# Performance work log

Hardware: AMD Instinct MI355X
Metric: run time of the kernel (lower is better)

Reference implementation:

```python
import jax, jax.numpy as jnp
import numpy as np

EPS = 1e-5

def bn(x, g, b, m, v):
    # inference-mode BatchNorm2d over channel dim
    return (x - m[None, :, None, None]) * jax.lax.rsqrt(v[None, :, None, None] + EPS) * g[None, :, None, None] + b[None, :, None, None]

def conv1x1(x, W, b=None):
    y = jnp.einsum('oc,bchw->bohw', W, x)
    return y + b[None, :, None, None] if b is not None else y

def forward(x, W3, b3, g1, b1, m1, v1, Wa, ba, g2, b2, m2, v2, Wq, bq, Wk, bk, Wv, bv, gam, Wg, bg, g3, b3n, m3, v3, Wf, bf, g4, b4, m4, v4, Wr, rs):
    B, C, H, Wd = x.shape
    N = H * Wd
    # conv branch: 3x3 conv + BN + ReLU
    y3 = jax.lax.conv_general_dilated(x, W3, (1, 1), ((1, 1), (1, 1)), dimension_numbers=('NCHW', 'OIHW', 'NCHW'))
    local = jax.nn.relu(bn(y3 + b3[None, :, None, None], g1, b1, m1, v1))
    # attn branch: 1x1 conv + BN + ReLU, then full-resolution attention
    a = jax.nn.relu(bn(conv1x1(x, Wa, ba), g2, b2, m2, v2))
    q = conv1x1(a, Wq, bq).reshape(B, -1, N)   # [B, C/8, N]
    k = conv1x1(a, Wk, bk).reshape(B, -1, N)   # [B, C/8, N]
    v = conv1x1(a, Wv, bv).reshape(B, -1, N)   # [B, C, N]
    att = jax.nn.softmax(jnp.einsum('bcn,bcm->bnm', q, k), axis=-1)  # [B, N, N], unscaled as in source
    o = jnp.einsum('bcm,bnm->bcn', v, att).reshape(a.shape)
    attn_feat = gam * o + a
    # gated fusion
    combined = jnp.concatenate([local, attn_feat], axis=1)
    gate = jax.nn.sigmoid(bn(conv1x1(combined, Wg, bg), g3, b3n, m3, v3))
    fused = gate * local + (1.0 - gate) * attn_feat
    out = jax.nn.relu(bn(conv1x1(jnp.concatenate([fused, combined], axis=1), Wf, bf), g4, b4, m4, v4))
    res = conv1x1(x, Wr)  # residual 1x1 conv, no bias (in != out channels)
    return out + rs * res

def setup_inputs() -> dict:
    B, Ci, Co, H, W_ = 4, 64, 128, 64, 64
    Cq = Co // 8
    ks = jax.random.split(jax.random.key(0), 24)
    def rn(i, s, sc=0.05):
        return jax.random.normal(ks[i], s, jnp.float32) * sc
    def var(i, c):
        return jax.random.uniform(ks[i], (c,), jnp.float32, 0.5, 1.5)
    ones = lambda c: jnp.ones((c,), jnp.float32)
    zeros = lambda c: jnp.zeros((c,), jnp.float32)
    return {
        'x': rn(0, (B, Ci, H, W_), 1.0),
        'W3': rn(1, (Co, Ci, 3, 3)), 'b3': rn(2, (Co,)),
        'g1': ones(Co), 'b1': zeros(Co), 'm1': rn(3, (Co,), 0.1), 'v1': var(4, Co),
        'Wa': rn(5, (Co, Ci)), 'ba': rn(6, (Co,)),
        'g2': ones(Co), 'b2': zeros(Co), 'm2': rn(7, (Co,), 0.1), 'v2': var(8, Co),
        'Wq': rn(9, (Cq, Co)), 'bq': rn(10, (Cq,)),
        'Wk': rn(11, (Cq, Co)), 'bk': rn(12, (Cq,)),
        'Wv': rn(13, (Co, Co)), 'bv': rn(14, (Co,)),
        'gam': jnp.array(0.5, jnp.float32),
        'Wg': rn(15, (Co, 2 * Co)), 'bg': rn(16, (Co,)),
        'g3': ones(Co), 'b3n': zeros(Co), 'm3': rn(17, (Co,), 0.1), 'v3': var(18, Co),
        'Wf': rn(19, (Co, 3 * Co)), 'bf': rn(20, (Co,)),
        'g4': ones(Co), 'b4': zeros(Co), 'm4': rn(21, (Co,), 0.1), 'v4': var(22, Co),
        'Wr': rn(23, (Co, Ci)),
        'rs': jnp.array(0.1, jnp.float32),
    }

def reference(x, W3, b3, g1, b1, m1, v1, Wa, ba, g2, b2, m2, v2, Wq, bq, Wk, bk, Wv, bv, gam, Wg, bg, g3, b3n, m3, v3, Wf, bf, g4, b4, m4, v4, Wr, rs):
    return forward(x, W3, b3, g1, b1, m1, v1, Wa, ba, g2, b2, m2, v2, Wq, bq, Wk, bk, Wv, bv, gam, Wg, bg, g3, b3n, m3, v3, Wf, bf, g4, b4, m4, v4, Wr, rs)
```

## Files before the change

kernel.cpp:

```cpp
#include <hip/hip_runtime.h>
#include <hip/hip_bf16.h>

#define CI_ 64
#define CO_ 128
#define NPIX 4096
#define CQ_ 16
#define EPS_ 1e-5f

typedef __attribute__((ext_vector_type(8))) __bf16 bf16x8;
typedef __attribute__((ext_vector_type(4))) __bf16 bf16x4;
typedef __attribute__((ext_vector_type(4))) float f32x4;

__global__ __launch_bounds__(256) void z_prepx(
    const float* __restrict__ x, __bf16* __restrict__ xT)
{
    __shared__ float tl[64][65];
    int b = blockIdx.x >> 6;
    int n0 = (blockIdx.x & 63) * 64;
    int tid = threadIdx.x;
    int nn = tid & 63, c4 = tid >> 6;
#pragma unroll
    for (int p = 0; p < 16; ++p) {
        int ci = p * 4 + c4;
        tl[ci][nn] = x[((size_t)b * CI_ + ci) * NPIX + n0 + nn];
    }
    __syncthreads();
#pragma unroll
    for (int p = 0; p < 2; ++p) {
        int idx = p * 256 + tid;
        int n = idx >> 3, cig = idx & 7;
        bf16x8 vv;
#pragma unroll
        for (int j = 0; j < 8; ++j) vv[j] = (__bf16)tl[cig * 8 + j][n];
        ((bf16x8*)xT)[((size_t)b * NPIX + n0 + n) * 8 + cig] = vv;
    }
}

__global__ __launch_bounds__(256) void z_prepw2(
    const float* __restrict__ W3, __bf16* __restrict__ Wt2,
    const float* __restrict__ Wg, const float* __restrict__ Wf, const float* __restrict__ Wr,
    const float* __restrict__ Wa, const float* __restrict__ Wq, const float* __restrict__ Wk,
    const float* __restrict__ Wv, __bf16* __restrict__ Wb)
{
    int i = blockIdx.x * 256 + threadIdx.x;
    if (i < 73728) {
        int co = i / 576;
        int r = i - co * 576;
        int tap = r >> 6;
        int ci = r & 63;
        Wt2[i] = (__bf16)W3[((size_t)co * CI_ + ci) * 9 + tap];
    }
    if (i < 118784) {
        float val;
        if (i < 32768) val = Wg[i];
        else if (i < 81920) val = Wf[i - 32768];
        else if (i < 90112) val = Wr[i - 81920];
        else if (i < 98304) val = Wa[i - 90112];
        else if (i < 100352) val = Wq[i - 98304];
        else if (i < 102400) val = Wk[i - 100352];
        else val = Wv[i - 102400];
        Wb[i] = (__bf16)val;
    }
}

__global__ __launch_bounds__(256) void z_mega(
    const __bf16* __restrict__ xT, const __bf16* __restrict__ Wb,
    const float* __restrict__ ba, const float* __restrict__ g2, const float* __restrict__ b2,
    const float* __restrict__ m2, const float* __restrict__ v2,
    const float* __restrict__ bq, const float* __restrict__ bk, const float* __restrict__ bv,
    float* __restrict__ a, float* __restrict__ q, __bf16* __restrict__ kT, __bf16* __restrict__ V2)
{
    __shared__ __align__(16) __bf16 an[16 * 128];
    int tid = threadIdx.x;
    int b = blockIdx.x >> 8;
    int n0 = (blockIdx.x & 255) * 16;
    int l = tid & 63, w = tid >> 6;
    int lm = l & 15, g = l >> 4;

    const __bf16* Wa2 = Wb + 90112;
    const __bf16* Wq2 = Wb + 98304;
    const __bf16* Wk2 = Wb + 100352;
    const __bf16* Wv2 = Wb + 102400;

    bf16x8 bx[2];
#pragma unroll
    for (int kc = 0; kc < 2; ++kc)
        bx[kc] = ((const bf16x8*)xT)[((size_t)b * NPIX + n0 + lm) * 8 + (kc * 4 + g)];
    f32x4 pa[2];
#pragma unroll
    for (int ct = 0; ct < 2; ++ct) {
#pragma unroll
        for (int r = 0; r < 4; ++r) pa[ct][r] = ba[w * 32 + ct * 16 + g * 4 + r];
#pragma unroll
        for (int kc = 0; kc < 2; ++kc) {
            bf16x8 afr = *(const bf16x8*)&Wa2[(size_t)(w * 32 + ct * 16 + lm) * 64 + kc * 32 + g * 8];
            pa[ct] = __builtin_amdgcn_mfma_f32_16x16x32_bf16(afr, bx[kc], pa[ct], 0, 0, 0);
        }
    }
#pragma unroll
    for (int ct = 0; ct < 2; ++ct) {
        bf16x4 pk;
#pragma unroll
        for (int r = 0; r < 4; ++r) {
            int co = w * 32 + ct * 16 + g * 4 + r;
            float sc = rsqrtf(v2[co] + EPS_) * g2[co];
            float sh = b2[co] - m2[co] * sc;
            float y = fmaxf(pa[ct][r] * sc + sh, 0.f);
            a[((size_t)b * CO_ + co) * NPIX + n0 + lm] = y;
            pk[r] = (__bf16)y;
        }
        int co8 = w * 4 + ct * 2 + (g >> 1);
        int ch = co8 ^ (lm & 7);
        *(bf16x4*)&an[lm * 128 + ch * 8 + (g & 1) * 4] = pk;
    }
    __syncthreads();

    bf16x8 bn[4];
#pragma unroll
    for (int kc = 0; kc < 4; ++kc) {
        int ch = (kc * 4 + g) ^ (lm & 7);
        bn[kc] = *(const bf16x8*)&an[lm * 128 + ch * 8];
    }
    f32x4 pv[2];
#pragma unroll
    for (int ct = 0; ct < 2; ++ct) {
#pragma unroll
        for (int r = 0; r < 4; ++r) pv[ct][r] = bv[w * 32 + ct * 16 + g * 4 + r];
#pragma unroll
        for (int kc = 0; kc < 4; ++kc) {
            bf16x8 afr = *(const bf16x8*)&Wv2[(size_t)(w * 32 + ct * 16 + lm) * 128 + kc * 32 + g * 8];
            pv[ct] = __builtin_amdgcn_mfma_f32_16x16x32_bf16(afr, bn[kc], pv[ct], 0, 0, 0);
        }
    }
    int n = n0 + lm;
#pragma unroll
    for (int ct = 0; ct < 2; ++ct)
#pragma unroll
        for (int r = 0; r < 4; ++r) {
            int c = w * 32 + ct * 16 + g * 4 + r;
            V2[(size_t)b * 524288 + (size_t)(n >> 3) * 1024 + c * 8 + (n & 7)] = (__bf16)pv[ct][r];
        }
    if (w == 0) {
        f32x4 pq;
#pragma unroll
        for (int r = 0; r < 4; ++r) pq[r] = bq[g * 4 + r];
#pragma unroll
        for (int kc = 0; kc < 4; ++kc) {
            bf16x8 afr = *(const bf16x8*)&Wq2[(size_t)lm * 128 + kc * 32 + g * 8];
            pq = __builtin_amdgcn_mfma_f32_16x16x32_bf16(afr, bn[kc], pq, 0, 0, 0);
        }
#pragma unroll
        for (int r = 0; r < 4; ++r)
            q[((size_t)b * CQ_ + g * 4 + r) * NPIX + n] = pq[r];
    } else if (w == 1) {
        f32x4 pk2;
#pragma unroll
        for (int r = 0; r < 4; ++r) pk2[r] = bk[g * 4 + r];
#pragma unroll
        for (int kc = 0; kc < 4; ++kc) {
            bf16x8 afr = *(const bf16x8*)&Wk2[(size_t)lm * 128 + kc * 32 + g * 8];
            pk2 = __builtin_amdgcn_mfma_f32_16x16x32_bf16(afr, bn[kc], pk2, 0, 0, 0);
        }
        bf16x4 kk;
#pragma unroll
        for (int r = 0; r < 4; ++r) kk[r] = (__bf16)pk2[r];
        *(bf16x4*)&kT[((size_t)b * NPIX + n) * CQ_ + g * 4] = kk;
    }
}

__global__ __launch_bounds__(256) void z_conv3mb(
    const __bf16* __restrict__ xT, const __bf16* __restrict__ Wt2,
    const float* __restrict__ b3, const float* __restrict__ g,
    const float* __restrict__ bb, const float* __restrict__ m,
    const float* __restrict__ v, __bf16* __restrict__ local_bf)
{
    __shared__ __align__(16) __bf16 xt[3 * 66 * 64];
    __shared__ __align__(16) __bf16 wt[32 * 576];
    __shared__ float scs[32], shs[32];

    int blk = blockIdx.x;
    int b = blk >> 8;
    int h = (blk >> 2) & 63;
    int cg = blk & 3;
    int co0 = cg * 32;
    int tid = threadIdx.x;
    int l = tid & 63;
    int nt = tid >> 6;
    int lm = l & 15, lh = l >> 4;

    if (tid < 32) {
        int co = co0 + tid;
        float scv = rsqrtf(v[co] + EPS_) * g[co];
        scs[tid] = scv;
        shs[tid] = (b3[co] - m[co]) * scv + bb[co];
    }

    const bf16x8* xs = (const bf16x8*)xT + (size_t)b * (NPIX * 8);
    for (int i = tid; i < 1584; i += 256) {
        int r = i / 528;
        int rem = i - r * 528;
        int c = rem >> 3;
        int cig = rem & 7;
        int hh = h + r - 1;
        int gc = c - 1;
        bf16x8 val;
#pragma unroll
        for (int j = 0; j < 8; ++j) val[j] = (__bf16)0.f;
        if ((unsigned)hh < 64u && (unsigned)gc < 64u)
            val = xs[(hh * 64 + gc) * 8 + cig];
        *(bf16x8*)&xt[(r * 66 + c) * 64 + ((cig ^ (c & 7)) * 8)] = val;
    }
    const bf16x8* wsrc = (const bf16x8*)Wt2 + (size_t)co0 * 72;
    for (int i = tid; i < 2304; i += 256) {
        int co = i / 72;
        int kc = i - co * 72;
        *(bf16x8*)&wt[co * 576 + ((kc ^ (co & 7)) * 8)] = wsrc[i];
    }
    __syncthreads();

    f32x4 acc0 = {0.f, 0.f, 0.f, 0.f};
    f32x4 acc1 = {0.f, 0.f, 0.f, 0.f};
#pragma unroll
    for (int tap = 0; tap < 9; ++tap) {
        int dh = tap / 3, dw = tap % 3;
#pragma unroll
        for (int ks = 0; ks < 2; ++ks) {
            int cig = ks * 4 + lh;
            int col = nt * 16 + lm + dw;
            bf16x8 bfr = *(const bf16x8*)&xt[(dh * 66 + col) * 64 + ((cig ^ (col & 7)) * 8)];
            int kcg = tap * 8 + cig;
            bf16x8 a0 = *(const bf16x8*)&wt[lm * 576 + ((kcg ^ (lm & 7)) * 8)];
            bf16x8 a1 = *(const bf16x8*)&wt[(16 + lm) * 576 + ((kcg ^ (lm & 7)) * 8)];
            acc0 = __builtin_amdgcn_mfma_f32_16x16x32_bf16(a0, bfr, acc0, 0, 0, 0);
            acc1 = __builtin_amdgcn_mfma_f32_16x16x32_bf16(a1, bfr, acc1, 0, 0, 0);
        }
    }

    size_t obase = (size_t)b * CO_ * NPIX + h * 64 + nt * 16 + lm;
#pragma unroll
    for (int r = 0; r < 4; ++r) {
        int cl0 = lh * 4 + r;
        float y0 = fmaxf(acc0[r] * scs[cl0] + shs[cl0], 0.f);
        local_bf[obase + (size_t)(co0 + cl0) * NPIX] = (__bf16)y0;
        int cl1 = 16 + cl0;
        float y1 = fmaxf(acc1[r] * scs[cl1] + shs[cl1], 0.f);
        local_bf[obase + (size_t)(co0 + cl1) * NPIX] = (__bf16)y1;
    }
}

__global__ __launch_bounds__(256) void z_attn8(
    const float* __restrict__ q, const __bf16* __restrict__ kT, const __bf16* __restrict__ V2,
    __bf16* __restrict__ o_part, float2* __restrict__ ml)
{
    __shared__ __align__(16) unsigned char smem[16896];
    __shared__ float wmaxA[4][16], wsumA[4][16], fsA[16];
    __shared__ float wmaxB[4][16], wsumB[4][16], fsB[16];
    __bf16* pA = (__bf16*)smem;
    __bf16* pB = (__bf16*)(smem + 8448);
    float* o_lds = (float*)smem;

    int tid = threadIdx.x;
    int b = blockIdx.x >> 8;
    int half = (blockIdx.x >> 7) & 1;
    int q0 = (blockIdx.x & 127) * 32;
    int l = tid & 63;
    int w = tid >> 6;
    int lm = l & 15;
    int g = l >> 4;

    bf16x8 qfA, qfB;
#pragma unroll
    for (int j = 0; j < 8; ++j) { qfA[j] = (__bf16)0.f; qfB[j] = (__bf16)0.f; }
    if (g < 2) {
#pragma unroll
        for (int j = 0; j < 8; ++j) {
            qfA[j] = (__bf16)q[((size_t)b * CQ_ + g * 8 + j) * NPIX + q0 + lm];
            qfB[j] = (__bf16)q[((size_t)b * CQ_ + g * 8 + j) * NPIX + q0 + 16 + lm];
        }
    }

    float mA = -1e30f, lA = 0.f, mB = -1e30f, lB = 0.f;
    f32x4 aA0 = {0.f,0.f,0.f,0.f}, aA1 = {0.f,0.f,0.f,0.f};
    f32x4 aB0 = {0.f,0.f,0.f,0.f}, aB1 = {0.f,0.f,0.f,0.f};
    int c0 = w * 32 + lm;
    int c1 = c0 + 16;
    const bf16x8* vbase = (const bf16x8*)V2 + (size_t)b * 65536;
    const __bf16* ktb = kT + (size_t)b * NPIX * CQ_;

    for (int t = 0; t < 8; ++t) {
        int m0 = half * 2048 + t * 256;
        {
            f32x4 sfr[4];
#pragma unroll
            for (int ms = 0; ms < 4; ++ms) {
                bf16x8 kf;
#pragma unroll
                for (int j = 0; j < 8; ++j) kf[j] = (__bf16)0.f;
                if (g < 2)
                    kf = *(const bf16x8*)&ktb[(size_t)(m0 + w * 64 + ms * 16 + lm) * CQ_ + g * 8];
                f32x4 zz = {0.f, 0.f, 0.f, 0.f};
                sfr[ms] = __builtin_amdgcn_mfma_f32_16x16x32_bf16(kf, qfA, zz, 0, 0, 0);
            }
            float pmax = -1e30f;
#pragma unroll
            for (int ms = 0; ms < 4; ++ms)
#pragma unroll
                for (int r = 0; r < 4; ++r) pmax = fmaxf(pmax, sfr[ms][r]);
            pmax = fmaxf(pmax, __shfl_xor(pmax, 16));
            pmax = fmaxf(pmax, __shfl_xor(pmax, 32));
            if (g == 0) wmaxA[w][lm] = pmax;
            __syncthreads();
            float tmax = fmaxf(fmaxf(wmaxA[0][lm], wmaxA[1][lm]), fmaxf(wmaxA[2][lm], wmaxA[3][lm]));
            float nm = fmaxf(mA, tmax);
            float f = __expf(mA - nm);
            mA = nm;
            if (w == 0 && g == 0) fsA[lm] = f;
            float psum = 0.f;
#pragma unroll
            for (int ms = 0; ms < 4; ++ms) {
                float p0 = __expf(sfr[ms][0] - nm);
                float p1 = __expf(sfr[ms][1] - nm);
                float p2 = __expf(sfr[ms][2] - nm);
                float p3 = __expf(sfr[ms][3] - nm);
                psum += (p0 + p1) + (p2 + p3);
                bf16x4 pk;
                pk[0] = (__bf16)p0; pk[1] = (__bf16)p1; pk[2] = (__bf16)p2; pk[3] = (__bf16)p3;
                *(bf16x4*)&pA[lm * 264 + w * 64 + ms * 16 + g * 4] = pk;
            }
            psum += __shfl_xor(psum, 16);
            psum += __shfl_xor(psum, 32);
            if (g == 0) wsumA[w][lm] = psum;
            __syncthreads();
            float tsum = (wsumA[0][lm] + wsumA[1][lm]) + (wsumA[2][lm] + wsumA[3][lm]);
            lA = lA * f + tsum;
        }
        {
            f32x4 sfr[4];
#pragma unroll
            for (int ms = 0; ms < 4; ++ms) {
                bf16x8 kf;
#pragma unroll
                for (int j = 0; j < 8; ++j) kf[j] = (__bf16)0.f;
                if (g < 2)
                    kf = *(const bf16x8*)&ktb[(size_t)(m0 + w * 64 + ms * 16 + lm) * CQ_ + g * 8];
                f32x4 zz = {0.f, 0.f, 0.f, 0.f};
                sfr[ms] = __builtin_amdgcn_mfma_f32_16x16x32_bf16(kf, qfB, zz, 0, 0, 0);
            }
            float pmax = -1e30f;
#pragma unroll
            for (int ms = 0; ms < 4; ++ms)
#pragma unroll
                for (int r = 0; r < 4; ++r) pmax = fmaxf(pmax, sfr[ms][r]);
            pmax = fmaxf(pmax, __shfl_xor(pmax, 16));
            pmax = fmaxf(pmax, __shfl_xor(pmax, 32));
            if (g == 0) wmaxB[w][lm] = pmax;
            __syncthreads();
            float tmax = fmaxf(fmaxf(wmaxB[0][lm], wmaxB[1][lm]), fmaxf(wmaxB[2][lm], wmaxB[3][lm]));
            float nm = fmaxf(mB, tmax);
            float f = __expf(mB - nm);
            mB = nm;
            if (w == 0 && g == 0) fsB[lm] = f;
            float psum = 0.f;
#pragma unroll
            for (int ms = 0; ms < 4; ++ms) {
                float p0 = __expf(sfr[ms][0] - nm);
                float p1 = __expf(sfr[ms][1] - nm);
                float p2 = __expf(sfr[ms][2] - nm);
                float p3 = __expf(sfr[ms][3] - nm);
                psum += (p0 + p1) + (p2 + p3);
                bf16x4 pk;
                pk[0] = (__bf16)p0; pk[1] = (__bf16)p1; pk[2] = (__bf16)p2; pk[3] = (__bf16)p3;
                *(bf16x4*)&pB[lm * 264 + w * 64 + ms * 16 + g * 4] = pk;
            }
            psum += __shfl_xor(psum, 16);
            psum += __shfl_xor(psum, 32);
            if (g == 0) wsumB[w][lm] = psum;
            __syncthreads();
            float tsum = (wsumB[0][lm] + wsumB[1][lm]) + (wsumB[2][lm] + wsumB[3][lm]);
            lB = lB * f + tsum;
        }
        {
            float fA0 = fsA[g * 4 + 0], fA1 = fsA[g * 4 + 1], fA2 = fsA[g * 4 + 2], fA3 = fsA[g * 4 + 3];
            float fB0 = fsB[g * 4 + 0], fB1 = fsB[g * 4 + 1], fB2 = fsB[g * 4 + 2], fB3 = fsB[g * 4 + 3];
            aA0[0] *= fA0; aA0[1] *= fA1; aA0[2] *= fA2; aA0[3] *= fA3;
            aA1[0] *= fA0; aA1[1] *= fA1; aA1[2] *= fA2; aA1[3] *= fA3;
            aB0[0] *= fB0; aB0[1] *= fB1; aB0[2] *= fB2; aB0[3] *= fB3;
            aB1[0] *= fB0; aB1[1] *= fB1; aB1[2] *= fB2; aB1[3] *= fB3;
#pragma unroll
            for (int ks = 0; ks < 8; ++ks) {
                int msv = (m0 >> 3) + ks * 4 + g;
                bf16x8 bf0 = vbase[msv * 128 + c0];
                bf16x8 bf1 = vbase[msv * 128 + c1];
                bf16x8 afA = *(const bf16x8*)&pA[lm * 264 + ks * 32 + g * 8];
                bf16x8 afB = *(const bf16x8*)&pB[lm * 264 + ks * 32 + g * 8];
                aA0 = __builtin_amdgcn_mfma_f32_16x16x32_bf16(afA, bf0, aA0, 0, 0, 0);
                aA1 = __builtin_amdgcn_mfma_f32_16x16x32_bf16(afA, bf1, aA1, 0, 0, 0);
                aB0 = __builtin_amdgcn_mfma_f32_16x16x32_bf16(afB, bf0, aB0, 0, 0, 0);
                aB1 = __builtin_amdgcn_mfma_f32_16x16x32_bf16(afB, bf1, aB1, 0, 0, 0);
            }
        }
    }

    __syncthreads();
#pragma unroll
    for (int r = 0; r < 4; ++r) {
        int qrow = g * 4 + r;
        o_lds[c0 * 17 + qrow] = aA0[r];
        o_lds[c1 * 17 + qrow] = aA1[r];
    }
    if (w == 0 && g == 0)
        ml[(size_t)(half * 4 + b) * NPIX + q0 + lm] = make_float2(mA, lA);
    __syncthreads();
    {
        int qi = tid & 15;
        float inv = 1.f / lA;
#pragma unroll
        for (int j = 0; j < 8; ++j) {
            int cc = (tid >> 4) + 16 * j;
            size_t idx = ((size_t)(half * 4 + b) * CO_ + cc) * NPIX + q0 + qi;
            o_part[idx] = (__bf16)(o_lds[cc * 17 + qi] * inv);
        }
    }
    __syncthreads();
#pragma unroll
    for (int r = 0; r < 4; ++r) {
        int qrow = g * 4 + r;
        o_lds[c0 * 17 + qrow] = aB0[r];
        o_lds[c1 * 17 + qrow] = aB1[r];
    }
    if (w == 0 && g == 0)
        ml[(size_t)(half * 4 + b) * NPIX + q0 + 16 + lm] = make_float2(mB, lB);
    __syncthreads();
    {
        int qi = tid & 15;
        float inv = 1.f / lB;
#pragma unroll
        for (int j = 0; j < 8; ++j) {
            int cc = (tid >> 4) + 16 * j;
            size_t idx = ((size_t)(half * 4 + b) * CO_ + cc) * NPIX + q0 + 16 + qi;
            o_part[idx] = (__bf16)(o_lds[cc * 17 + qi] * inv);
        }
    }
}

__global__ __launch_bounds__(256) void z_fuseout3(
    const __bf16* __restrict__ local_bf, const __bf16* __restrict__ o_part,
    const float2* __restrict__ ml, const float* __restrict__ a,
    const float* __restrict__ gamp, const __bf16* __restrict__ xT,
    const __bf16* __restrict__ Wb,
    const float* __restrict__ bg, const float* __restrict__ g3, const float* __restrict__ b3n,
    const float* __restrict__ m3, const float* __restrict__ v3,
    const float* __restrict__ bfb, const float* __restrict__ g4, const float* __restrict__ b4,
    const float* __restrict__ m4, const float* __restrict__ v4,
    const float* __restrict__ rsp, float* __restrict__ out)
{
    __shared__ __align__(16) unsigned char smem[32768 + 4096];
    __shared__ float wA[32], wB[32];
    __bf16* sb2 = (__bf16*)smem;
    __bf16* sxT = (__bf16*)(smem + 28672);

    int tid = threadIdx.x;
    int b = blockIdx.x >> 7;
    int n0 = (blockIdx.x & 127) * 32;

    if (tid < 32) {
        float2 m1 = ml[(size_t)b * NPIX + n0 + tid];
        float2 m2 = ml[(size_t)(4 + b) * NPIX + n0 + tid];
        float mm = fmaxf(m1.x, m2.x);
        float w1 = m1.y * __expf(m1.x - mm);
        float w2 = m2.y * __expf(m2.x - mm);
        float inv = 1.f / (w1 + w2);
        wA[tid] = w1 * inv;
        wB[tid] = w2 * inv;
    }
    __syncthreads();

    float gam = gamp[0];
#pragma unroll
    for (int p = 0; p < 4; ++p) {
        int idx = p * 256 + tid;
        int c = idx >> 3, j = idx & 7;
        bf16x4 lv = *(const bf16x4*)&local_bf[((size_t)b * CO_ + c) * NPIX + n0 + j * 4];
        bf16x4 o1 = *(const bf16x4*)&o_part[((size_t)b * CO_ + c) * NPIX + n0 + j * 4];
        bf16x4 o2 = *(const bf16x4*)&o_part[((size_t)(4 + b) * CO_ + c) * NPIX + n0 + j * 4];
        float av[4];
        *(float4*)av = *(const float4*)(a + ((size_t)b * CO_ + c) * NPIX + n0 + j * 4);
#pragma unroll
        for (int e = 0; e < 4; ++e) {
            int n = j * 4 + e;
            int k1 = 128 + c, k2 = 256 + c;
            sb2[n * 448 + (((k1 >> 3) ^ (n & 7)) << 3) + (k1 & 7)] = lv[e];
            float o = (float)o1[e] * wA[n] + (float)o2[e] * wB[n];
            sb2[n * 448 + (((k2 >> 3) ^ (n & 7)) << 3) + (k2 & 7)] = (__bf16)(gam * o + av[e]);
        }
    }
#pragma unroll
    for (int p = 0; p < 2; ++p) {
        int idx = p * 256 + tid;
        int n = idx >> 3, cig = idx & 7;
        bf16x8 vv = ((const bf16x8*)xT)[((size_t)b * NPIX + n0 + n) * 8 + cig];
        *(bf16x8*)&sxT[n * 64 + ((cig ^ (n & 7)) << 3)] = vv;
    }
    __syncthreads();

    int l = tid & 63, w = tid >> 6;
    int lm = l & 15, g = l >> 4;
    int co0 = w * 32;
    int t7 = lm & 7;

    f32x4 p1[2][2];
#pragma unroll
    for (int cs = 0; cs < 2; ++cs) {
        float bv = bg[co0 + cs * 16 + lm];
#pragma unroll
        for (int ns = 0; ns < 2; ++ns) {
            p1[ns][cs][0] = bv; p1[ns][cs][1] = bv; p1[ns][cs][2] = bv; p1[ns][cs][3] = bv;
        }
    }
    const __bf16* Wg2 = Wb;
#pragma unroll
    for (int kc = 0; kc < 8; ++kc) {
        int ch = (16 + kc * 4 + g) ^ t7;
        bf16x8 a0 = *(const bf16x8*)&sb2[lm * 448 + ch * 8];
        bf16x8 a1 = *(const bf16x8*)&sb2[(16 + lm) * 448 + ch * 8];
        bf16x8 b0 = *(const bf16x8*)&Wg2[(size_t)(co0 + lm) * 256 + kc * 32 + g * 8];
        bf16x8 b1 = *(const bf16x8*)&Wg2[(size_t)(co0 + 16 + lm) * 256 + kc * 32 + g * 8];
        p1[0][0] = __builtin_amdgcn_mfma_f32_16x16x32_bf16(a0, b0, p1[0][0], 0, 0, 0);
        p1[0][1] = __builtin_amdgcn_mfma_f32_16x16x32_bf16(a0, b1, p1[0][1], 0, 0, 0);
        p1[1][0] = __builtin_amdgcn_mfma_f32_16x16x32_bf16(a1, b0, p1[1][0], 0, 0, 0);
        p1[1][1] = __builtin_amdgcn_mfma_f32_16x16x32_bf16(a1, b1, p1[1][1], 0, 0, 0);
    }
#pragma unroll
    for (int cs = 0; cs < 2; ++cs) {
        int co = co0 + cs * 16 + lm;
        float sc3 = rsqrtf(v3[co] + EPS_) * g3[co];
        float sh3 = b3n[co] - m3[co] * sc3;
        int kl = 128 + co, ka = 256 + co;
#pragma unroll
        for (int ns = 0; ns < 2; ++ns)
#pragma unroll
            for (int r = 0; r < 4; ++r) {
                int n = ns * 16 + g * 4 + r;
                float z = p1[ns][cs][r] * sc3 + sh3;
                float gate = 1.f / (1.f + __expf(-z));
                float lv = (float)sb2[n * 448 + (((kl >> 3) ^ (n & 7)) << 3) + (kl & 7)];
                float av = (float)sb2[n * 448 + (((ka >> 3) ^ (n & 7)) << 3) + (ka & 7)];
                float fu = gate * lv + (1.f - gate) * av;
                sb2[n * 448 + (((co >> 3) ^ (n & 7)) << 3) + (co & 7)] = (__bf16)fu;
            }
    }
    __syncthreads();

    f32x4 p2[2][2], pr[2][2];
#pragma unroll
    for (int cs = 0; cs < 2; ++cs) {
        float bv = bfb[co0 + cs * 16 + lm];
#pragma unroll
        for (int ns = 0; ns < 2; ++ns) {
            p2[ns][cs][0] = bv; p2[ns][cs][1] = bv; p2[ns][cs][2] = bv; p2[ns][cs][3] = bv;
            pr[ns][cs] = (f32x4){0.f, 0.f, 0.f, 0.f};
        }
    }
    const __bf16* Wf2 = Wb + 32768;
    const __bf16* Wr2 = Wb + 81920;
#pragma unroll
    for (int kc = 0; kc < 12; ++kc) {
        int ch = (kc * 4 + g) ^ t7;
        bf16x8 a0 = *(const bf16x8*)&sb2[lm * 448 + ch * 8];
        bf16x8 a1 = *(const bf16x8*)&sb2[(16 + lm) * 448 + ch * 8];
        bf16x8 b0 = *(const bf16x8*)&Wf2[(size_t)(co0 + lm) * 384 + kc * 32 + g * 8];
        bf16x8 b1 = *(const bf16x8*)&Wf2[(size_t)(co0 + 16 + lm) * 384 + kc * 32 + g * 8];
        p2[0][0] = __builtin_amdgcn_mfma_f32_16x16x32_bf16(a0, b0, p2[0][0], 0, 0, 0);
        p2[0][1] = __builtin_amdgcn_mfma_f32_16x16x32_bf16(a0, b1, p2[0][1], 0, 0, 0);
        p2[1][0] = __builtin_amdgcn_mfma_f32_16x16x32_bf16(a1, b0, p2[1][0], 0, 0, 0);
        p2[1][1] = __builtin_amdgcn_mfma_f32_16x16x32_bf16(a1, b1, p2[1][1], 0, 0, 0);
    }
#pragma unroll
    for (int kc = 0; kc < 2; ++kc) {
        int ch = (kc * 4 + g) ^ t7;
        bf16x8 a0 = *(const bf16x8*)&sxT[lm * 64 + ch * 8];
        bf16x8 a1 = *(const bf16x8*)&sxT[(16 + lm) * 64 + ch * 8];
        bf16x8 b0 = *(const bf16x8*)&Wr2[(size_t)(co0 + lm) * 64 + kc * 32 + g * 8];
        bf16x8 b1 = *(const bf16x8*)&Wr2[(size_t)(co0 + 16 + lm) * 64 + kc * 32 + g * 8];
        pr[0][0] = __builtin_amdgcn_mfma_f32_16x16x32_bf16(a0, b0, pr[0][0], 0, 0, 0);
        pr[0][1] = __builtin_amdgcn_mfma_f32_16x16x32_bf16(a0, b1, pr[0][1], 0, 0, 0);
        pr[1][0] = __builtin_amdgcn_mfma_f32_16x16x32_bf16(a1, b0, pr[1][0], 0, 0, 0);
        pr[1][1] = __builtin_amdgcn_mfma_f32_16x16x32_bf16(a1, b1, pr[1][1], 0, 0, 0);
    }
    __syncthreads();

    float* o_lds = (float*)smem;
    float rsv = rsp[0];
#pragma unroll
    for (int cs = 0; cs < 2; ++cs) {
        int co = co0 + cs * 16 + lm;
        float sc4 = rsqrtf(v4[co] + EPS_) * g4[co];
        float sh4 = b4[co] - m4[co] * sc4;
#pragma unroll
        for (int ns = 0; ns < 2; ++ns)
#pragma unroll
            for (int r = 0; r < 4; ++r) {
                int n = ns * 16 + g * 4 + r;
                float o = fmaxf(p2[ns][cs][r] * sc4 + sh4, 0.f) + rsv * pr[ns][cs][r];
                o_lds[co * 36 + n] = o;
            }
    }
    __syncthreads();
    {
        int c = tid >> 1, h = tid & 1;
#pragma unroll
        for (int j2 = 0; j2 < 4; ++j2) {
            float4 vv = *(float4*)&o_lds[c * 36 + h * 16 + j2 * 4];
            *(float4*)(out + ((size_t)b * CO_ + c) * NPIX + n0 + h * 16 + j2 * 4) = vv;
        }
    }
}

extern "C" void kernel_launch(void* const* d_in, const int* in_sizes, int n_in,
                              void* d_out, int out_size, void* d_ws, size_t ws_size,
                              hipStream_t stream) {
    const float* x   = (const float*)d_in[0];
    const float* W3  = (const float*)d_in[1];
    const float* b3  = (const float*)d_in[2];
    const float* g1  = (const float*)d_in[3];
    const float* b1  = (const float*)d_in[4];
    const float* m1  = (const float*)d_in[5];
    const float* v1  = (const float*)d_in[6];
    const float* Wa  = (const float*)d_in[7];
    const float* ba  = (const float*)d_in[8];
    const float* g2  = (const float*)d_in[9];
    const float* b2  = (const float*)d_in[10];
    const float* m2  = (const float*)d_in[11];
    const float* v2  = (const float*)d_in[12];
    const float* Wq  = (const float*)d_in[13];
    const float* bq  = (const float*)d_in[14];
    const float* Wk  = (const float*)d_in[15];
    const float* bk  = (const float*)d_in[16];
    const float* Wv  = (const float*)d_in[17];
    const float* bv  = (const float*)d_in[18];
    const float* gam = (const float*)d_in[19];
    const float* Wg  = (const float*)d_in[20];
    const float* bg  = (const float*)d_in[21];
    const float* g3  = (const float*)d_in[22];
    const float* b3n = (const float*)d_in[23];
    const float* m3  = (const float*)d_in[24];
    const float* v3  = (const float*)d_in[25];
    const float* Wf  = (const float*)d_in[26];
    const float* bfb = (const float*)d_in[27];
    const float* g4  = (const float*)d_in[28];
    const float* b4  = (const float*)d_in[29];
    const float* m4  = (const float*)d_in[30];
    const float* v4  = (const float*)d_in[31];
    const float* Wr  = (const float*)d_in[32];
    const float* rs  = (const float*)d_in[33];

    float* ws      = (float*)d_ws;
    float* a_      = ws;
    __bf16* local_bf = (__bf16*)(ws + 2097152);
    __bf16* V2     = (__bf16*)(ws + 3145728);
    float* q       = ws + 4194304;
    __bf16* kT     = (__bf16*)(ws + 4456448);
    __bf16* xT     = (__bf16*)(ws + 4587520);
    __bf16* Wt2    = (__bf16*)(ws + 5111808);
    __bf16* Wb     = (__bf16*)(ws + 5152768);
    __bf16* o_part = (__bf16*)(ws + 5214208);
    float2* ml     = (float2*)(ws + 7311360);

    float* out = (float*)d_out;

    z_prepx<<<256, 256, 0, stream>>>(x, xT);
    z_prepw2<<<464, 256, 0, stream>>>(W3, Wt2, Wg, Wf, Wr, Wa, Wq, Wk, Wv, Wb);
    z_mega<<<1024, 256, 0, stream>>>(xT, Wb, ba, g2, b2, m2, v2, bq, bk, bv, a_, q, kT, V2);
    z_attn8<<<1024, 256, 0, stream>>>(q, kT, V2, o_part, ml);
    z_conv3mb<<<1024, 256, 0, stream>>>(xT, Wt2, b3, g1, b1, m1, v1, local_bf);
    z_fuseout3<<<512, 256, 0, stream>>>(local_bf, o_part, ml, a_, gam, xT, Wb,
                                        bg, g3, b3n, m3, v3, bfb, g4, b4, m4, v4, rs, out);
}
```

Before: 109.6 us.

## Use two-pass softmax with precomputed row max and store Q as bf16 transposed

The attention kernel now runs a first pass over all keys in its half to compute the exact row maximum of QK^T. A second pass computes the exponentials, accumulates P·V and sums the probabilities without any online rescaling. This removes the per-tile max/sum block reductions, most syncthreads and the accumulator rescale multiplies. The price is computing the QK^T MFMAs twice. Q is also written by the projection kernel as bf16 in a pixel-major layout, so each lane loads its fragment with one vector load instead of 16 strided fp32 loads.

```diff
diff --git a/kernel.cpp b/kernel.cpp
--- a/kernel.cpp
+++ b/kernel.cpp
@@ -68,7 +68,7 @@
     const float* __restrict__ ba, const float* __restrict__ g2, const float* __restrict__ b2,
     const float* __restrict__ m2, const float* __restrict__ v2,
     const float* __restrict__ bq, const float* __restrict__ bk, const float* __restrict__ bv,
-    float* __restrict__ a, float* __restrict__ q, __bf16* __restrict__ kT, __bf16* __restrict__ V2)
+    float* __restrict__ a, __bf16* __restrict__ qT, __bf16* __restrict__ kT, __bf16* __restrict__ V2)
 {
     __shared__ __align__(16) __bf16 an[16 * 128];
     int tid = threadIdx.x;
@@ -149,9 +149,10 @@
             bf16x8 afr = *(const bf16x8*)&Wq2[(size_t)lm * 128 + kc * 32 + g * 8];
             pq = __builtin_amdgcn_mfma_f32_16x16x32_bf16(afr, bn[kc], pq, 0, 0, 0);
         }
-#pragma unroll
-        for (int r = 0; r < 4; ++r)
-            q[((size_t)b * CQ_ + g * 4 + r) * NPIX + n] = pq[r];
+        bf16x4 qq;
+#pragma unroll
+        for (int r = 0; r < 4; ++r) qq[r] = (__bf16)pq[r];
+        *(bf16x4*)&qT[((size_t)b * NPIX + n) * CQ_ + g * 4] = qq;
     } else if (w == 1) {
         f32x4 pk2;
 #pragma unroll
@@ -248,13 +249,12 @@
     }
 }
 
-__global__ __launch_bounds__(256) void z_attn8(
-    const float* __restrict__ q, const __bf16* __restrict__ kT, const __bf16* __restrict__ V2,
+__global__ __launch_bounds__(256) void z_attn9(
+    const __bf16* __restrict__ qT, const __bf16* __restrict__ kT, const __bf16* __restrict__ V2,
     __bf16* __restrict__ o_part, float2* __restrict__ ml)
 {
     __shared__ __align__(16) unsigned char smem[16896];
-    __shared__ float wmaxA[4][16], wsumA[4][16], fsA[16];
-    __shared__ float wmaxB[4][16], wsumB[4][16], fsB[16];
+    __shared__ float wredA[4][16], wredB[4][16];
     __bf16* pA = (__bf16*)smem;
     __bf16* pB = (__bf16*)(smem + 8448);
     float* o_lds = (float*)smem;
@@ -271,137 +271,100 @@
     bf16x8 qfA, qfB;
 #pragma unroll
     for (int j = 0; j < 8; ++j) { qfA[j] = (__bf16)0.f; qfB[j] = (__bf16)0.f; }
+    const __bf16* qtb = qT + (size_t)b * NPIX * CQ_;
     if (g < 2) {
-#pragma unroll
-        for (int j = 0; j < 8; ++j) {
-            qfA[j] = (__bf16)q[((size_t)b * CQ_ + g * 8 + j) * NPIX + q0 + lm];
-            qfB[j] = (__bf16)q[((size_t)b * CQ_ + g * 8 + j) * NPIX + q0 + 16 + lm];
-        }
-    }
-
-    float mA = -1e30f, lA = 0.f, mB = -1e30f, lB = 0.f;
+        qfA = *(const bf16x8*)&qtb[(size_t)(q0 + lm) * CQ_ + g * 8];
+        qfB = *(const bf16x8*)&qtb[(size_t)(q0 + 16 + lm) * CQ_ + g * 8];
+    }
+
+    const bf16x8* vbase = (const bf16x8*)V2 + (size_t)b * 65536;
+    const __bf16* ktb = kT + (size_t)b * NPIX * CQ_;
+
+    float mxA = -1e30f, mxB = -1e30f;
+    for (int t = 0; t < 8; ++t) {
+        int m0 = half * 2048 + t * 256;
+#pragma unroll
+        for (int ms = 0; ms < 4; ++ms) {
+            bf16x8 kf;
+#pragma unroll
+            for (int j = 0; j < 8; ++j) kf[j] = (__bf16)0.f;
+            if (g < 2)
+                kf = *(const bf16x8*)&ktb[(size_t)(m0 + w * 64 + ms * 16 + lm) * CQ_ + g * 8];
+            f32x4 zz = {0.f, 0.f, 0.f, 0.f};
+            f32x4 sA = __builtin_amdgcn_mfma_f32_16x16x32_bf16(kf, qfA, zz, 0, 0, 0);
+            f32x4 sB = __builtin_amdgcn_mfma_f32_16x16x32_bf16(kf, qfB, zz, 0, 0, 0);
+#pragma unroll
+            for (int r = 0; r < 4; ++r) {
+                mxA = fmaxf(mxA, sA[r]);
+                mxB = fmaxf(mxB, sB[r]);
+            }
+        }
+    }
+    mxA = fmaxf(mxA, __shfl_xor(mxA, 16));
+    mxA = fmaxf(mxA, __shfl_xor(mxA, 32));
+    mxB = fmaxf(mxB, __shfl_xor(mxB, 16));
+    mxB = fmaxf(mxB, __shfl_xor(mxB, 32));
+    if (g == 0) { wredA[w][lm] = mxA; wredB[w][lm] = mxB; }
+    __syncthreads();
+    float MA = fmaxf(fmaxf(wredA[0][lm], wredA[1][lm]), fmaxf(wredA[2][lm], wredA[3][lm]));
+    float MB = fmaxf(fmaxf(wredB[0][lm], wredB[1][lm]), fmaxf(wredB[2][lm], wredB[3][lm]));
+
     f32x4 aA0 = {0.f,0.f,0.f,0.f}, aA1 = {0.f,0.f,0.f,0.f};
     f32x4 aB0 = {0.f,0.f,0.f,0.f}, aB1 = {0.f,0.f,0.f,0.f};
+    float sumA = 0.f, sumB = 0.f;
     int c0 = w * 32 + lm;
     int c1 = c0 + 16;
-    const bf16x8* vbase = (const bf16x8*)V2 + (size_t)b * 65536;
-    const __bf16* ktb = kT + (size_t)b * NPIX * CQ_;
 
     for (int t = 0; t < 8; ++t) {
         int m0 = half * 2048 + t * 256;
-        {
-            f32x4 sfr[4];
-#pragma unroll
-            for (int ms = 0; ms < 4; ++ms) {
-                bf16x8 kf;
-#pragma unroll
-                for (int j = 0; j < 8; ++j) kf[j] = (__bf16)0.f;
-                if (g < 2)
-                    kf = *(const bf16x8*)&ktb[(size_t)(m0 + w * 64 + ms * 16 + lm) * CQ_ + g * 8];
-                f32x4 zz = {0.f, 0.f, 0.f, 0.f};
-                sfr[ms] = __builtin_amdgcn_mfma_f32_16x16x32_bf16(kf, qfA, zz, 0, 0, 0);
-            }
-            float pmax = -1e30f;
-#pragma unroll
-            for (int ms = 0; ms < 4; ++ms)
-#pragma unroll
-                for (int r = 0; r < 4; ++r) pmax = fmaxf(pmax, sfr[ms][r]);
-            pmax = fmaxf(pmax, __shfl_xor(pmax, 16));
-            pmax = fmaxf(pmax, __shfl_xor(pmax, 32));
-            if (g == 0) wmaxA[w][lm] = pmax;
-            __syncthreads();
-            float tmax = fmaxf(fmaxf(wmaxA[0][lm], wmaxA[1][lm]), fmaxf(wmaxA[2][lm], wmaxA[3][lm]));
-            float nm = fmaxf(mA, tmax);
-            float f = __expf(mA - nm);
-            mA = nm;
-            if (w == 0 && g == 0) fsA[lm] = f;
-            float psum = 0.f;
-#pragma unroll
-            for (int ms = 0; ms < 4; ++ms) {
-                float p0 = __expf(sfr[ms][0] - nm);
-                float p1 = __expf(sfr[ms][1] - nm);
-                float p2 = __expf(sfr[ms][2] - nm);
-                float p3 = __expf(sfr[ms][3] - nm);
-                psum += (p0 + p1) + (p2 + p3);
-                bf16x4 pk;
-                pk[0] = (__bf16)p0; pk[1] = (__bf16)p1; pk[2] = (__bf16)p2; pk[3] = (__bf16)p3;
-                *(bf16x4*)&pA[lm * 264 + w * 64 + ms * 16 + g * 4] = pk;
-            }
-            psum += __shfl_xor(psum, 16);
-            psum += __shfl_xor(psum, 32);
-            if (g == 0) wsumA[w][lm] = psum;
-            __syncthreads();
-            float tsum = (wsumA[0][lm] + wsumA[1][lm]) + (wsumA[2][lm] + wsumA[3][lm]);
-            lA = lA * f + tsum;
-        }
-        {
-            f32x4 sfr[4];
-#pragma unroll
-            for (int ms = 0; ms < 4; ++ms) {
-                bf16x8 kf;
-#pragma unroll
-                for (int j = 0; j < 8; ++j) kf[j] = (__bf16)0.f;
-                if (g < 2)
-                    kf = *(const bf16x8*)&ktb[(size_t)(m0 + w * 64 + ms * 16 + lm) * CQ_ + g * 8];
-                f32x4 zz = {0.f, 0.f, 0.f, 0.f};
-                sfr[ms] = __builtin_amdgcn_mfma_f32_16x16x32_bf16(kf, qfB, zz, 0, 0, 0);
-            }
-            float pmax = -1e30f;
-#pragma unroll
-            for (int ms = 0; ms < 4; ++ms)
-#pragma unroll
-                for (int r = 0; r < 4; ++r) pmax = fmaxf(pmax, sfr[ms][r]);
-            pmax = fmaxf(pmax, __shfl_xor(pmax, 16));
-            pmax = fmaxf(pmax, __shfl_xor(pmax, 32));
-            if (g == 0) wmaxB[w][lm] = pmax;
-            __syncthreads();
-            float tmax = fmaxf(fmaxf(wmaxB[0][lm], wmaxB[1][lm]), fmaxf(wmaxB[2][lm], wmaxB[3][lm]));
-            float nm = fmaxf(mB, tmax);
-            float f = __expf(mB - nm);
-            mB = nm;
-            if (w == 0 && g == 0) fsB[lm] = f;
-            float psum = 0.f;
-#pragma unroll
-            for (int ms = 0; ms < 4; ++ms) {
-                float p0 = __expf(sfr[ms][0] - nm);
-                float p1 = __expf(sfr[ms][1] - nm);
-                float p2 = __expf(sfr[ms][2] - nm);
-                float p3 = __expf(sfr[ms][3] - nm);
-                psum += (p0 + p1) + (p2 + p3);
-                bf16x4 pk;
-                pk[0] = (__bf16)p0; pk[1] = (__bf16)p1; pk[2] = (__bf16)p2; pk[3] = (__bf16)p3;
-                *(bf16x4*)&pB[lm * 264 + w * 64 + ms * 16 + g * 4] = pk;
-            }
-            psum += __shfl_xor(psum, 16);
-            psum += __shfl_xor(psum, 32);
-            if (g == 0) wsumB[w][lm] = psum;
-            __syncthreads();
-            float tsum = (wsumB[0][lm] + wsumB[1][lm]) + (wsumB[2][lm] + wsumB[3][lm]);
-            lB = lB * f + tsum;
-        }
-        {
-            float fA0 = fsA[g * 4 + 0], fA1 = fsA[g * 4 + 1], fA2 = fsA[g * 4 + 2], fA3 = fsA[g * 4 + 3];
-            float fB0 = fsB[g * 4 + 0], fB1 = fsB[g * 4 + 1], fB2 = fsB[g * 4 + 2], fB3 = fsB[g * 4 + 3];
-            aA0[0] *= fA0; aA0[1] *= fA1; aA0[2] *= fA2; aA0[3] *= fA3;
-            aA1[0] *= fA0; aA1[1] *= fA1; aA1[2] *= fA2; aA1[3] *= fA3;
-            aB0[0] *= fB0; aB0[1] *= fB1; aB0[2] *= fB2; aB0[3] *= fB3;
-            aB1[0] *= fB0; aB1[1] *= fB1; aB1[2] *= fB2; aB1[3] *= fB3;
-#pragma unroll
-            for (int ks = 0; ks < 8; ++ks) {
-                int msv = (m0 >> 3) + ks * 4 + g;
-                bf16x8 bf0 = vbase[msv * 128 + c0];
-                bf16x8 bf1 = vbase[msv * 128 + c1];
-                bf16x8 afA = *(const bf16x8*)&pA[lm * 264 + ks * 32 + g * 8];
-                bf16x8 afB = *(const bf16x8*)&pB[lm * 264 + ks * 32 + g * 8];
-                aA0 = __builtin_amdgcn_mfma_f32_16x16x32_bf16(afA, bf0, aA0, 0, 0, 0);
-                aA1 = __builtin_amdgcn_mfma_f32_16x16x32_bf16(afA, bf1, aA1, 0, 0, 0);
-                aB0 = __builtin_amdgcn_mfma_f32_16x16x32_bf16(afB, bf0, aB0, 0, 0, 0);
-                aB1 = __builtin_amdgcn_mfma_f32_16x16x32_bf16(afB, bf1, aB1, 0, 0, 0);
-            }
-        }
-    }
-
-    __syncthreads();
+#pragma unroll
+        for (int ms = 0; ms < 4; ++ms) {
+            bf16x8 kf;
+#pragma unroll
+            for (int j = 0; j < 8; ++j) kf[j] = (__bf16)0.f;
+            if (g < 2)
+                kf = *(const bf16x8*)&ktb[(size_t)(m0 + w * 64 + ms * 16 + lm) * CQ_ + g * 8];
+            f32x4 zz = {0.f, 0.f, 0.f, 0.f};
+            f32x4 sA = __builtin_amdgcn_mfma_f32_16x16x32_bf16(kf, qfA, zz, 0, 0, 0);
+            f32x4 sB = __builtin_amdgcn_mfma_f32_16x16x32_bf16(kf, qfB, zz, 0, 0, 0);
+            float a0 = __expf(sA[0] - MA), a1 = __expf(sA[1] - MA);
+            float a2 = __expf(sA[2] - MA), a3 = __expf(sA[3] - MA);
+            sumA += (a0 + a1) + (a2 + a3);
+            bf16x4 pkA;
+            pkA[0] = (__bf16)a0; pkA[1] = (__bf16)a1; pkA[2] = (__bf16)a2; pkA[3] = (__bf16)a3;
+            *(bf16x4*)&pA[lm * 264 + w * 64 + ms * 16 + g * 4] = pkA;
+            float b0 = __expf(sB[0] - MB), b1 = __expf(sB[1] - MB);
+            float b2 = __expf(sB[2] - MB), b3 = __expf(sB[3] - MB);
+            sumB += (b0 + b1) + (b2 + b3);
+            bf16x4 pkB;
+            pkB[0] = (__bf16)b0; pkB[1] = (__bf16)b1; pkB[2] = (__bf16)b2; pkB[3] = (__bf16)b3;
+            *(bf16x4*)&pB[lm * 264 + w * 64 + ms * 16 + g * 4] = pkB;
+        }
+        __syncthreads();
+#pragma unroll
+        for (int ks = 0; ks < 8; ++ks) {
+            int msv = (m0 >> 3) + ks * 4 + g;
+            bf16x8 bf0 = vbase[msv * 128 + c0];
+            bf16x8 bf1 = vbase[msv * 128 + c1];
+            bf16x8 afA = *(const bf16x8*)&pA[lm * 264 + ks * 32 + g * 8];
+            bf16x8 afB = *(const bf16x8*)&pB[lm * 264 + ks * 32 + g * 8];
+            aA0 = __builtin_amdgcn_mfma_f32_16x16x32_bf16(afA, bf0, aA0, 0, 0, 0);
+            aA1 = __builtin_amdgcn_mfma_f32_16x16x32_bf16(afA, bf1, aA1, 0, 0, 0);
+            aB0 = __builtin_amdgcn_mfma_f32_16x16x32_bf16(afB, bf0, aB0, 0, 0, 0);
+            aB1 = __builtin_amdgcn_mfma_f32_16x16x32_bf16(afB, bf1, aB1, 0, 0, 0);
+        }
+        __syncthreads();
+    }
+
+    sumA += __shfl_xor(sumA, 16);
+    sumA += __shfl_xor(sumA, 32);
+    sumB += __shfl_xor(sumB, 16);
+    sumB += __shfl_xor(sumB, 32);
+    if (g == 0) { wredA[w][lm] = sumA; wredB[w][lm] = sumB; }
+    __syncthreads();
+    float lA = (wredA[0][lm] + wredA[1][lm]) + (wredA[2][lm] + wredA[3][lm]);
+    float lB = (wredB[0][lm] + wredB[1][lm]) + (wredB[2][lm] + wredB[3][lm]);
+
 #pragma unroll
     for (int r = 0; r < 4; ++r) {
         int qrow = g * 4 + r;
@@ -409,7 +372,7 @@
         o_lds[c1 * 17 + qrow] = aA1[r];
     }
     if (w == 0 && g == 0)
-        ml[(size_t)(half * 4 + b) * NPIX + q0 + lm] = make_float2(mA, lA);
+        ml[(size_t)(half * 4 + b) * NPIX + q0 + lm] = make_float2(MA, lA);
     __syncthreads();
     {
         int qi = tid & 15;
@@ -429,7 +392,7 @@
         o_lds[c1 * 17 + qrow] = aB1[r];
     }
     if (w == 0 && g == 0)
-        ml[(size_t)(half * 4 + b) * NPIX + q0 + 16 + lm] = make_float2(mB, lB);
+        ml[(size_t)(half * 4 + b) * NPIX + q0 + 16 + lm] = make_float2(MB, lB);
     __syncthreads();
     {
         int qi = tid & 15;
@@ -658,20 +621,20 @@
     float* a_      = ws;
     __bf16* local_bf = (__bf16*)(ws + 2097152);
     __bf16* V2     = (__bf16*)(ws + 3145728);
-    float* q       = ws + 4194304;
-    __bf16* kT     = (__bf16*)(ws + 4456448);
-    __bf16* xT     = (__bf16*)(ws + 4587520);
-    __bf16* Wt2    = (__bf16*)(ws + 5111808);
-    __bf16* Wb     = (__bf16*)(ws + 5152768);
-    __bf16* o_part = (__bf16*)(ws + 5214208);
-    float2* ml     = (float2*)(ws + 7311360);
+    __bf16* qT     = (__bf16*)(ws + 4194304);
+    __bf16* kT     = (__bf16*)(ws + 4325376);
+    __bf16* xT     = (__bf16*)(ws + 4456448);
+    __bf16* Wt2    = (__bf16*)(ws + 4980736);
+    __bf16* Wb     = (__bf16*)(ws + 5017600);
+    __bf16* o_part = (__bf16*)(ws + 5076992);
+    float2* ml     = (float2*)(ws + 7174144);
 
     float* out = (float*)d_out;
 
     z_prepx<<<256, 256, 0, stream>>>(x, xT);
     z_prepw2<<<464, 256, 0, stream>>>(W3, Wt2, Wg, Wf, Wr, Wa, Wq, Wk, Wv, Wb);
-    z_mega<<<1024, 256, 0, stream>>>(xT, Wb, ba, g2, b2, m2, v2, bq, bk, bv, a_, q, kT, V2);
-    z_attn8<<<1024, 256, 0, stream>>>(q, kT, V2, o_part, ml);
+    z_mega<<<1024, 256, 0, stream>>>(xT, Wb, ba, g2, b2, m2, v2, bq, bk, bv, a_, qT, kT, V2);
+    z_attn9<<<1024, 256, 0, stream>>>(qT, kT, V2, o_part, ml);
     z_conv3mb<<<1024, 256, 0, stream>>>(xT, Wt2, b3, g1, b1, m1, v1, local_bf);
     z_fuseout3<<<512, 256, 0, stream>>>(local_bf, o_part, ml, a_, gam, xT, Wb,
                                         bg, g3, b3n, m3, v3, bfb, g4, b4, m4, v4, rs, out);
```

Result: faster. 106.5 us (-2.8%).
